# Optimization experiments

Measured on AMD Instinct MI355X. Metric: run time of the kernel, lower is better.

Reference implementation:

```python
import jax, jax.numpy as jnp
import numpy as np

B, T, D, H, L = 128, 512, 512, 512, 256


def setup_inputs() -> dict:
    key = jax.random.key(0)
    ks = jax.random.split(key, 7)
    lim = 1.0 / np.sqrt(H)
    u = lambda k, shape, lo: jax.random.uniform(k, shape, jnp.float32, -lo, lo)
    x = jax.random.normal(ks[0], (B, T, D), dtype=jnp.float32)
    Wih = u(ks[1], (3 * H, D), lim)
    Whh = u(ks[2], (3 * H, H), lim)
    b = u(ks[3], (3 * H,), lim)
    bn = u(ks[4], (H,), lim)
    lim_l = 1.0 / np.sqrt(H)
    Wlin = u(ks[5], (2 * L, H), lim_l)
    blin = u(ks[6], (2 * L,), lim_l)
    return {"x": x, "Wih": Wih, "Whh": Whh, "b": b, "bn": bn, "Wlin": Wlin, "blin": blin}


def reference(x, Wih, Whh, b, bn, Wlin, blin):
    # x: (B, T, D). Batched GRU recurrence over time via lax.scan.
    def step(h, xt):
        ig = xt @ Wih.T + b           # (B, 3H)
        hg = h @ Whh.T                # (B, 3H)
        ir, iz, inn = jnp.split(ig, 3, axis=-1)
        hr, hz, hn = jnp.split(hg, 3, axis=-1)
        r = jax.nn.sigmoid(ir + hr)
        z = jax.nn.sigmoid(iz + hz)
        n = jnp.tanh(inn + r * (hn + bn))
        h_new = (1.0 - z) * n + z * h
        return h_new, None

    xs = jnp.swapaxes(x, 0, 1)        # (T, B, D)
    h0 = jnp.zeros((x.shape[0], Whh.shape[1]), dtype=x.dtype)
    h_final, _ = jax.lax.scan(step, h0, xs)
    out = h_final @ Wlin.T + blin     # (B, 2L)
    mu, logvar = jnp.split(out, 2, axis=-1)
    return (mu, logvar)
```

## Files before the change

kernel.cpp:

```cpp
#include <hip/hip_runtime.h>
#include <stdint.h>


typedef short short8 __attribute__((ext_vector_type(8)));
typedef float f32x4 __attribute__((ext_vector_type(4)));
typedef int int4v __attribute__((ext_vector_type(4)));

#define NB 128
#define NT 512
#define ND 512
#define NH 512
#define NG 1536
#define HSLOT (NB * NH)

__device__ __forceinline__ unsigned short f2bf(float f) {
  union { float f; unsigned u; } v; v.f = f;
  unsigned r = v.u + 0x7fffu + ((v.u >> 16) & 1u);
  return (unsigned short)(r >> 16);
}
__device__ __forceinline__ float bf2f(unsigned short u) {
  union { unsigned u; float f; } v; v.u = ((unsigned)u) << 16; return v.f;
}
__device__ __forceinline__ float sigmoid_f(float x) {
  float e = __builtin_amdgcn_exp2f(-1.4426950408889634f * x);
  return __builtin_amdgcn_rcpf(1.0f + e);
}
__device__ __forceinline__ float tanh_f(float x) {
  float e = __builtin_amdgcn_exp2f(2.8853900817779268f * x);
  return 1.0f - 2.0f * __builtin_amdgcn_rcpf(1.0f + e);
}
__device__ __forceinline__ short8 pack8(float4 a, float4 b) {
  short8 s;
  s[0] = (short)f2bf(a.x); s[1] = (short)f2bf(a.y);
  s[2] = (short)f2bf(a.z); s[3] = (short)f2bf(a.w);
  s[4] = (short)f2bf(b.x); s[5] = (short)f2bf(b.y);
  s[6] = (short)f2bf(b.z); s[7] = (short)f2bf(b.w);
  return s;
}

__device__ __forceinline__ void issue4(const unsigned short* r0,
                                       const unsigned short* r1,
                                       const unsigned short* r2,
                                       const unsigned short* r3,
                                       int4v (&v)[4]) {
  asm volatile(
      "global_load_dwordx4 %0, %4, off sc0 sc1\n\t"
      "global_load_dwordx4 %1, %5, off sc0 sc1\n\t"
      "global_load_dwordx4 %2, %6, off sc0 sc1\n\t"
      "global_load_dwordx4 %3, %7, off sc0 sc1"
      : "=&v"(v[0]), "=&v"(v[1]), "=&v"(v[2]), "=&v"(v[3])
      : "v"(r0), "v"(r1), "v"(r2), "v"(r3) : "memory");
}

__device__ __forceinline__ void wait4(int4v (&v)[4]) {
  asm volatile("s_waitcnt vmcnt(0)"
               : "+v"(v[0]), "+v"(v[1]), "+v"(v[2]), "+v"(v[3]) :: "memory");
}

__device__ __forceinline__ int4v load16_s(const unsigned short* p) {
  int4v v;
  asm volatile("global_load_dwordx4 %0, %1, off sc0 sc1\n\t"
               "s_waitcnt vmcnt(0)"
               : "=v"(v) : "v"(p) : "memory");
  return v;
}

__device__ __forceinline__ void store8_nd(unsigned short* p, unsigned long long v) {
  asm volatile("global_store_dwordx2 %0, %1, off sc0 sc1"
               :: "v"(p), "v"(v) : "memory");
}

__device__ __forceinline__ void store16_s(unsigned short* p, int4v v) {
  asm volatile("global_store_dwordx4 %0, %1, off sc0 sc1"
               :: "v"(p), "v"(v) : "memory");
}

__device__ __forceinline__ unsigned poll_s(const unsigned* p) {
  unsigned f;
  asm volatile("global_load_dword %0, %1, off sc0 sc1\n\t"
               "s_waitcnt vmcnt(0)" : "=v"(f) : "v"(p) : "memory");
  return f;
}

__device__ __forceinline__ unsigned pkmax(unsigned a, unsigned b) {
  unsigned d;
  asm("v_pk_max_u16 %0, %1, %2" : "=v"(d) : "v"(a), "v"(b));
  return d;
}
__device__ __forceinline__ bool has_sent(int4v v) {
  unsigned m = pkmax(pkmax((unsigned)v[0], (unsigned)v[1]),
                     pkmax((unsigned)v[2], (unsigned)v[3]));
  return ((m & 0xFFFFu) == 0xFFFFu) || ((m >> 16) == 0xFFFFu);
}

__global__ __launch_bounds__(256) void cvt_bf16(
    const float* __restrict__ in, unsigned short* __restrict__ out, int n8) {
  int i = blockIdx.x * blockDim.x + threadIdx.x;
  const int stride = gridDim.x * blockDim.x;
  for (; i < n8; i += stride) {
    float4 a = ((const float4*)in)[2 * i];
    float4 b = ((const float4*)in)[2 * i + 1];
    *(short8*)&out[(size_t)i * 8] = pack8(a, b);
  }
}

__global__ __launch_bounds__(256) void ig_gemm(
    const float* __restrict__ x, const float* __restrict__ Wih,
    const float* __restrict__ bias, unsigned short* __restrict__ IG) {
  __shared__ unsigned short As[128 * 40];
  __shared__ unsigned short Bs[128 * 40];
  const int tid = threadIdx.x;
  const int bn = blockIdx.x, bm = blockIdx.y;
  const int lane = tid & 63, w = tid >> 6;
  const int wm = w >> 1, wn = w & 1;
  const int l15 = lane & 15, q = lane >> 4;

  f32x4 acc[4][4] = {};

  for (int kt = 0; kt < 16; ++kt) {
    __syncthreads();
#pragma unroll
    for (int j = 0; j < 4; ++j) {
      int fi = tid + 256 * j;
      int row = fi >> 3, kq = fi & 7;
      float4 v = *(const float4*)(x + (size_t)(bm * 128 + row) * ND + kt * 32 + kq * 4);
      ushort4 s = {f2bf(v.x), f2bf(v.y), f2bf(v.z), f2bf(v.w)};
      *(ushort4*)&As[row * 40 + kq * 4] = s;
    }
#pragma unroll
    for (int j = 0; j < 4; ++j) {
      int fi = tid + 256 * j;
      int row = fi >> 3, kq = fi & 7;
      float4 v = *(const float4*)(Wih + (size_t)(bn * 128 + row) * ND + kt * 32 + kq * 4);
      ushort4 s = {f2bf(v.x), f2bf(v.y), f2bf(v.z), f2bf(v.w)};
      *(ushort4*)&Bs[row * 40 + kq * 4] = s;
    }
    __syncthreads();

    short8 af[4], bf[4];
#pragma unroll
    for (int tm = 0; tm < 4; ++tm)
      af[tm] = *(const short8*)&As[(wm * 64 + tm * 16 + l15) * 40 + q * 8];
#pragma unroll
    for (int tn = 0; tn < 4; ++tn)
      bf[tn] = *(const short8*)&Bs[(wn * 64 + tn * 16 + l15) * 40 + q * 8];
#pragma unroll
    for (int tm = 0; tm < 4; ++tm)
#pragma unroll
      for (int tn = 0; tn < 4; ++tn)
        acc[tm][tn] = __builtin_amdgcn_mfma_f32_16x16x32_bf16(af[tm], bf[tn], acc[tm][tn], 0, 0, 0);
  }

#pragma unroll
  for (int tm = 0; tm < 4; ++tm) {
#pragma unroll
    for (int tn = 0; tn < 4; ++tn) {
      int col = bn * 128 + wn * 64 + tn * 16 + l15;
      float bb = bias[col];
#pragma unroll
      for (int i = 0; i < 4; ++i) {
        int row = bm * 128 + wm * 64 + tm * 16 + q * 4 + i;
        IG[(size_t)row * NG + col] = f2bf(acc[tm][tn][i] + bb);
      }
    }
  }
}

template <bool USE_IG>
__device__ __forceinline__ void gru_body(
    const float* __restrict__ x, const float* __restrict__ Wih,
    const float* __restrict__ Whh, const float* __restrict__ bias,
    const float* __restrict__ bn, const unsigned short* __restrict__ IG,
    unsigned short* __restrict__ hbuf, float* __restrict__ hfin,
    const unsigned* __restrict__ qcnt,
    unsigned short* hs, unsigned short* ts, int bid) {
  const int tid = threadIdx.x;
  const int lane = tid & 63;
  const int w = tid >> 6;
  const int l15 = lane & 15, q = lane >> 4;
  const int g = bid & 7, c = bid >> 3;
  const int col = c * 64 + w * 16 + l15;
  const int erow = g * 16 + q * 4;
  const int mrow = g * 16 + l15;

  short8 bfr[3][16];
#pragma unroll
  for (int gt = 0; gt < 3; ++gt) {
    const float* src = Whh + (size_t)(gt * NH + col) * NH + q * 8;
#pragma unroll
    for (int kk = 0; kk < 16; ++kk) {
      float4 v0 = *(const float4*)(src + kk * 32);
      float4 v1 = *(const float4*)(src + kk * 32 + 4);
      bfr[gt][kk] = pack8(v0, v1);
    }
  }

  float bi_r = 0.f, bi_z = 0.f, bi_n = 0.f;
  if (!USE_IG) {
    bi_r = bias[col];
    bi_z = bias[NH + col];
    bi_n = bias[2 * NH + col];
  }
  const float bnv = bn[col];

  float hreg[4] = {0.f, 0.f, 0.f, 0.f};

  const int frow = tid >> 4;
  const int j2 = tid & 15;
  const int fr7 = frow & 7;
  const size_t rowoff = (size_t)(g * 16 + frow) * NH;
  const int e0 = ((j2) ^ fr7) << 3;
  const int e1 = ((j2 + 16) ^ fr7) << 3;
  const int e2 = ((32 + j2) ^ fr7) << 3;
  const int e3 = ((48 + j2) ^ fr7) << 3;

  const int srow = tid >> 4;
  const int scol = (tid & 15) * 4;
  const size_t cell_off = (size_t)(g * 16 + srow) * NH + c * 64 + scol;

  int4v v[4];
  issue4(hbuf + rowoff + e0, hbuf + rowoff + e1,
         hbuf + rowoff + e2, hbuf + rowoff + e3, v);

  for (int t = 0; t < NT; ++t) {
    unsigned short* hnxt  = hbuf + (size_t)((t + 1) & 3) * HSLOT;
    unsigned short* hsent = hbuf + (size_t)((t + 2) & 3) * HSLOT;
    const unsigned short* hrow = hbuf + (size_t)(t & 3) * HSLOT + rowoff;

    if (USE_IG && qcnt != nullptr && (t & 127) == 0) {
      if (tid == 0) {
        const unsigned* qp = qcnt + (t >> 7);
        unsigned f = poll_s(qp);
        while (f < 1536u) f = poll_s(qp);
      }
      __syncthreads();
    }

    float igr[4], igz[4], ign[4];
    if (USE_IG) {
#pragma unroll
      for (int i = 0; i < 4; ++i) {
        const size_t base = ((size_t)(erow + i) * NT + t) * NG + col;
        igr[i] = bf2f(IG[base]);
        igz[i] = bf2f(IG[base + NH]);
        ign[i] = bf2f(IG[base + 2 * NH]);
      }
    }

    wait4(v);
    if (t > 0) {
      while (has_sent(v[0])) v[0] = load16_s(hrow + e0);
      while (has_sent(v[1])) v[1] = load16_s(hrow + e1);
      while (has_sent(v[2])) v[2] = load16_s(hrow + e2);
      while (has_sent(v[3])) v[3] = load16_s(hrow + e3);
    }
    *(int4v*)&hs[frow * 512 + (j2 << 3)] = v[0];
    *(int4v*)&hs[frow * 512 + ((j2 + 16) << 3)] = v[1];
    *(int4v*)&hs[frow * 512 + ((32 + j2) << 3)] = v[2];
    *(int4v*)&hs[frow * 512 + ((48 + j2) << 3)] = v[3];
    __syncthreads();

    if (t + 2 < NT) store8_nd(hsent + cell_off, 0xFFFFFFFFFFFFFFFFull);

    f32x4 ar = {0.f, 0.f, 0.f, 0.f};
    f32x4 az = {0.f, 0.f, 0.f, 0.f};
    f32x4 an = {0.f, 0.f, 0.f, 0.f};
    f32x4 ai = {0.f, 0.f, 0.f, 0.f};
    const int abase = l15 * 512;
    const int ar7 = (l15 & 7) << 3;
#pragma unroll
    for (int kk = 0; kk < 16; ++kk) {
      short8 afk = *(const short8*)&hs[abase + ((kk * 32 + q * 8) ^ ar7)];
      ar = __builtin_amdgcn_mfma_f32_16x16x32_bf16(afk, bfr[0][kk], ar, 0, 0, 0);
      az = __builtin_amdgcn_mfma_f32_16x16x32_bf16(afk, bfr[1][kk], az, 0, 0, 0);
      an = __builtin_amdgcn_mfma_f32_16x16x32_bf16(afk, bfr[2][kk], an, 0, 0, 0);
      if (!USE_IG) {
        const float* xp = x + ((size_t)mrow * NT + t) * ND + kk * 32 + q * 8;
        short8 xa = pack8(*(const float4*)xp, *(const float4*)(xp + 4));
#pragma unroll
        for (int gt = 0; gt < 3; ++gt) {
          const float* wp = Wih + (size_t)(gt * NH + col) * ND + kk * 32 + q * 8;
          short8 wf = pack8(*(const float4*)wp, *(const float4*)(wp + 4));
          if (gt == 0) ar = __builtin_amdgcn_mfma_f32_16x16x32_bf16(xa, wf, ar, 0, 0, 0);
          if (gt == 1) az = __builtin_amdgcn_mfma_f32_16x16x32_bf16(xa, wf, az, 0, 0, 0);
          if (gt == 2) ai = __builtin_amdgcn_mfma_f32_16x16x32_bf16(xa, wf, ai, 0, 0, 0);
        }
      }
    }

    unsigned short sv[4];
#pragma unroll
    for (int i = 0; i < 4; ++i) {
      float xr = USE_IG ? (ar[i] + igr[i]) : (ar[i] + bi_r);
      float xz = USE_IG ? (az[i] + igz[i]) : (az[i] + bi_z);
      float xin = USE_IG ? ign[i] : (ai[i] + bi_n);
      float r = sigmoid_f(xr);
      float z = sigmoid_f(xz);
      float n = tanh_f(xin + r * (an[i] + bnv));
      float hn2 = (1.f - z) * n + z * hreg[i];
      hreg[i] = hn2;
      sv[i] = f2bf(hn2);
      if (t == NT - 1) hfin[(size_t)(erow + i) * NH + col] = hn2;
    }

    if (t != NT - 1) {
#pragma unroll
      for (int i = 0; i < 4; ++i)
        ts[(q * 4 + i) * 64 + w * 16 + l15] = sv[i];
      asm volatile("s_waitcnt vmcnt(0)" ::: "memory");
      __syncthreads();
      store8_nd(hnxt + cell_off,
                *(const unsigned long long*)&ts[srow * 64 + scol]);
      issue4(hnxt + rowoff + e0, hnxt + rowoff + e1,
             hnxt + rowoff + e2, hnxt + rowoff + e3, v);
    }
  }
}

template <bool USE_IG>
__global__ __launch_bounds__(256, 1) void gru_rec(
    const float* __restrict__ x, const float* __restrict__ Wih,
    const float* __restrict__ Whh, const float* __restrict__ bias,
    const float* __restrict__ bn, const unsigned short* __restrict__ IG,
    unsigned short* __restrict__ hbuf, float* __restrict__ hfin) {
  __shared__ __align__(16) unsigned short hs[16 * 512];
  __shared__ __align__(16) unsigned short ts[16 * 64];
  gru_body<USE_IG>(x, Wih, Whh, bias, bn, IG, hbuf, hfin, nullptr,
                   hs, ts, blockIdx.x);
}

__global__ __launch_bounds__(256, 1) void fused_gru_ig(
    const float* __restrict__ Whh, const float* __restrict__ bn,
    const unsigned short* __restrict__ xb, const unsigned short* __restrict__ wb,
    const float* __restrict__ bias, unsigned short* __restrict__ IG,
    unsigned short* __restrict__ hbuf, float* __restrict__ hfin,
    unsigned* __restrict__ qcnt) {
  __shared__ __align__(16) unsigned short hs[16 * 512];
  __shared__ __align__(16) unsigned short ts[16 * 64];
  __shared__ __align__(16) unsigned short As[128 * 40];
  __shared__ __align__(16) unsigned short Bs[128 * 40];
  __shared__ __align__(16) unsigned short Ts[128 * 128];

  const int bid = blockIdx.x;
  const int tid = threadIdx.x;

  if (bid < 64) {
    gru_body<true>(nullptr, nullptr, Whh, bias, bn, IG, hbuf, hfin, qcnt,
                   hs, ts, bid);
    return;
  }

  const int lane = tid & 63, w = tid >> 6;
  const int wm = w >> 1, wn = w & 1;
  const int l15 = lane & 15, q = lane >> 4;

  for (int tile = bid - 64; tile < 6144; tile += 192) {
    const int qq = tile / 1536;
    const int r = tile - qq * 1536;
    const int bmq = r / 12, bnn = r - bmq * 12;
    const int bm = bmq * 4 + qq;

    f32x4 acc[4][4] = {};

    for (int kt = 0; kt < 16; ++kt) {
      __syncthreads();
#pragma unroll
      for (int j = 0; j < 2; ++j) {
        int gi = tid + 256 * j;
        int row = gi >> 2, kq = gi & 3;
        *(short8*)&As[row * 40 + kq * 8] =
            *(const short8*)(xb + (size_t)(bm * 128 + row) * ND + kt * 32 + kq * 8);
      }
#pragma unroll
      for (int j = 0; j < 2; ++j) {
        int gi = tid + 256 * j;
        int row = gi >> 2, kq = gi & 3;
        *(short8*)&Bs[row * 40 + kq * 8] =
            *(const short8*)(wb + (size_t)(bnn * 128 + row) * ND + kt * 32 + kq * 8);
      }
      __syncthreads();

      short8 af[4], bf[4];
#pragma unroll
      for (int tm = 0; tm < 4; ++tm)
        af[tm] = *(const short8*)&As[(wm * 64 + tm * 16 + l15) * 40 + q * 8];
#pragma unroll
      for (int tn = 0; tn < 4; ++tn)
        bf[tn] = *(const short8*)&Bs[(wn * 64 + tn * 16 + l15) * 40 + q * 8];
#pragma unroll
      for (int tm = 0; tm < 4; ++tm)
#pragma unroll
        for (int tn = 0; tn < 4; ++tn)
          acc[tm][tn] = __builtin_amdgcn_mfma_f32_16x16x32_bf16(af[tm], bf[tn], acc[tm][tn], 0, 0, 0);
    }

#pragma unroll
    for (int tm = 0; tm < 4; ++tm) {
#pragma unroll
      for (int tn = 0; tn < 4; ++tn) {
        int cl = wn * 64 + tn * 16 + l15;
        float bb = bias[bnn * 128 + cl];
#pragma unroll
        for (int i = 0; i < 4; ++i) {
          int rl = wm * 64 + tm * 16 + q * 4 + i;
          Ts[rl * 128 + cl] = f2bf(acc[tm][tn][i] + bb);
        }
      }
    }
    __syncthreads();
#pragma unroll
    for (int j = 0; j < 8; ++j) {
      int gi = tid + 256 * j;
      int row = gi >> 4, c16 = gi & 15;
      store16_s(IG + (size_t)(bm * 128 + row) * NG + bnn * 128 + c16 * 8,
                *(const int4v*)&Ts[row * 128 + c16 * 8]);
    }
    asm volatile("s_waitcnt vmcnt(0)" ::: "memory");
    __syncthreads();
    if (tid == 0) atomicAdd(qcnt + qq, 1u);
  }
}

__global__ __launch_bounds__(256) void final_linear(
    const float* __restrict__ hfin, const float* __restrict__ Wlin,
    const float* __restrict__ blin, float* __restrict__ out) {
  __shared__ float sh[16 * 516];
  const int tid = threadIdx.x;
  const int b0 = blockIdx.y * 16, o0 = blockIdx.x * 16;

  for (int j = tid; j < 16 * 128; j += 256) {
    int row = j >> 7, kq = j & 127;
    *(float4*)&sh[row * 516 + kq * 4] =
        *(const float4*)(hfin + (size_t)(b0 + row) * NH + kq * 4);
  }
  __syncthreads();

  const int bi = tid & 15, oi = tid >> 4;
  const int o = o0 + oi;
  const float4* wp = (const float4*)(Wlin + (size_t)o * NH);
  float4 a4 = {0.f, 0.f, 0.f, 0.f};
  for (int k4 = 0; k4 < 128; ++k4) {
    float4 wv = wp[k4];
    float4 hv = *(const float4*)&sh[bi * 516 + k4 * 4];
    a4.x += wv.x * hv.x; a4.y += wv.y * hv.y;
    a4.z += wv.z * hv.z; a4.w += wv.w * hv.w;
  }
  float v = a4.x + a4.y + a4.z + a4.w + blin[o];
  int b = b0 + bi;
  if (o < 256) out[b * 256 + o] = v;
  else out[32768 + b * 256 + (o - 256)] = v;
}

extern "C" void kernel_launch(void* const* d_in, const int* in_sizes, int n_in,
                              void* d_out, int out_size, void* d_ws, size_t ws_size,
                              hipStream_t stream) {
  const float* x    = (const float*)d_in[0];
  const float* Wih  = (const float*)d_in[1];
  const float* Whh  = (const float*)d_in[2];
  const float* bias = (const float*)d_in[3];
  const float* bn   = (const float*)d_in[4];
  const float* Wlin = (const float*)d_in[5];
  const float* blin = (const float*)d_in[6];
  float* out = (float*)d_out;

  char* ws = (char*)d_ws;
  unsigned short* hbuf = (unsigned short*)ws;
  float* hfin          = (float*)(ws + 4 * 131072);
  unsigned* qcnt       = (unsigned*)(ws + 4 * 131072 + 262144);
  unsigned short* IG   = (unsigned short*)(ws + 4 * 131072 + 262144 + 1024);
  const size_t need_min = 4 * 131072 + 262144 + 1024;
  const size_t need_ig  = need_min + (size_t)NB * NT * NG * 2;
  const size_t need_bf  = need_ig + 67108864ull + 1572864ull;
  unsigned short* xb = (unsigned short*)(ws + need_ig);
  unsigned short* wb = (unsigned short*)(ws + need_ig + 67108864ull);
  if (ws_size < need_min) return;

  hipMemsetAsync(ws, 0, 131072, stream);
  hipMemsetAsync(ws + 131072, 0xFF, 3 * 131072, stream);
  hipMemsetAsync(ws + 4 * 131072 + 262144, 0, 1024, stream);

  const bool useIG = (ws_size >= need_ig);
  const bool useBF = (ws_size >= need_bf);
  if (useIG && useBF) {
    cvt_bf16<<<2048, 256, 0, stream>>>(x, xb, (NB * NT * ND) / 8);
    cvt_bf16<<<384, 256, 0, stream>>>(Wih, wb, (NG * ND) / 8);
    fused_gru_ig<<<256, 256, 0, stream>>>(Whh, bn, xb, wb, bias, IG, hbuf,
                                          hfin, qcnt);
  } else if (useIG) {
    ig_gemm<<<dim3(12, 512), 256, 0, stream>>>(x, Wih, bias, IG);
    gru_rec<true><<<64, 256, 0, stream>>>(x, Wih, Whh, bias, bn, IG, hbuf, hfin);
  } else {
    gru_rec<false><<<64, 256, 0, stream>>>(x, Wih, Whh, bias, bn, nullptr, hbuf, hfin);
  }
  final_linear<<<dim3(32, 8), 256, 0, stream>>>(hfin, Wlin, blin, out);
}
```

Before: 1.899 ms.

## Drop bf16 pre-conversion kernels and prefill first IG quarter with all blocks

Removes the separate fp32-to-bf16 conversion kernels for x and Wih, so the fused kernel now loads fp32 and converts while staging tiles into shared memory. Before the recurrence starts, all 256 blocks cooperatively compute the first quarter of the input-gate GEMM. The remaining quarters are then produced by the 192 non-recurrent blocks while the 64 recurrent blocks run. This cuts two kernel launches and a pass over x through memory, at the cost of doubling global load bytes inside the GEMM tiles and delaying the recurrence start until the first quarter is done.

After: 1.918 ms. No clear change (+1.0%).

```diff
diff --git a/kernel.cpp b/kernel.cpp
--- a/kernel.cpp
+++ b/kernel.cpp
@@ -93,17 +93,6 @@
   return ((m & 0xFFFFu) == 0xFFFFu) || ((m >> 16) == 0xFFFFu);
 }
 
-__global__ __launch_bounds__(256) void cvt_bf16(
-    const float* __restrict__ in, unsigned short* __restrict__ out, int n8) {
-  int i = blockIdx.x * blockDim.x + threadIdx.x;
-  const int stride = gridDim.x * blockDim.x;
-  for (; i < n8; i += stride) {
-    float4 a = ((const float4*)in)[2 * i];
-    float4 b = ((const float4*)in)[2 * i + 1];
-    *(short8*)&out[(size_t)i * 8] = pack8(a, b);
-  }
-}
-
 __global__ __launch_bounds__(256) void ig_gemm(
     const float* __restrict__ x, const float* __restrict__ Wih,
     const float* __restrict__ bias, unsigned short* __restrict__ IG) {
@@ -164,6 +153,77 @@
       }
     }
   }
+}
+
+__device__ __forceinline__ void ig_tile(
+    const float* __restrict__ x, const float* __restrict__ Wih,
+    const float* __restrict__ bias, unsigned short* __restrict__ IG,
+    unsigned* __restrict__ qcnt, int bm, int bnn, int qq,
+    unsigned short* As, unsigned short* Bs, unsigned short* Ts, int tid) {
+  const int lane = tid & 63, w = tid >> 6;
+  const int wm = w >> 1, wn = w & 1;
+  const int l15 = lane & 15, q = lane >> 4;
+
+  f32x4 acc[4][4] = {};
+
+  for (int kt = 0; kt < 16; ++kt) {
+    __syncthreads();
+#pragma unroll
+    for (int j = 0; j < 4; ++j) {
+      int fi = tid + 256 * j;
+      int row = fi >> 3, kq = fi & 7;
+      float4 v = *(const float4*)(x + (size_t)(bm * 128 + row) * ND + kt * 32 + kq * 4);
+      ushort4 s = {f2bf(v.x), f2bf(v.y), f2bf(v.z), f2bf(v.w)};
+      *(ushort4*)&As[row * 40 + kq * 4] = s;
+    }
+#pragma unroll
+    for (int j = 0; j < 4; ++j) {
+      int fi = tid + 256 * j;
+      int row = fi >> 3, kq = fi & 7;
+      float4 v = *(const float4*)(Wih + (size_t)(bnn * 128 + row) * ND + kt * 32 + kq * 4);
+      ushort4 s = {f2bf(v.x), f2bf(v.y), f2bf(v.z), f2bf(v.w)};
+      *(ushort4*)&Bs[row * 40 + kq * 4] = s;
+    }
+    __syncthreads();
+
+    short8 af[4], bf[4];
+#pragma unroll
+    for (int tm = 0; tm < 4; ++tm)
+      af[tm] = *(const short8*)&As[(wm * 64 + tm * 16 + l15) * 40 + q * 8];
+#pragma unroll
+    for (int tn = 0; tn < 4; ++tn)
+      bf[tn] = *(const short8*)&Bs[(wn * 64 + tn * 16 + l15) * 40 + q * 8];
+#pragma unroll
+    for (int tm = 0; tm < 4; ++tm)
+#pragma unroll
+      for (int tn = 0; tn < 4; ++tn)
+        acc[tm][tn] = __builtin_amdgcn_mfma_f32_16x16x32_bf16(af[tm], bf[tn], acc[tm][tn], 0, 0, 0);
+  }
+
+#pragma unroll
+  for (int tm = 0; tm < 4; ++tm) {
+#pragma unroll
+    for (int tn = 0; tn < 4; ++tn) {
+      int cl = wn * 64 + tn * 16 + l15;
+      float bb = bias[bnn * 128 + cl];
+#pragma unroll
+      for (int i = 0; i < 4; ++i) {
+        int rl = wm * 64 + tm * 16 + q * 4 + i;
+        Ts[rl * 128 + cl] = f2bf(acc[tm][tn][i] + bb);
+      }
+    }
+  }
+  __syncthreads();
+#pragma unroll
+  for (int j = 0; j < 8; ++j) {
+    int gi = tid + 256 * j;
+    int row = gi >> 4, c16 = gi & 15;
+    store16_s(IG + (size_t)(bm * 128 + row) * NG + bnn * 128 + c16 * 8,
+              *(const int4v*)&Ts[row * 128 + c16 * 8]);
+  }
+  asm volatile("s_waitcnt vmcnt(0)" ::: "memory");
+  __syncthreads();
+  if (tid == 0) atomicAdd(qcnt + qq, 1u);
 }
 
 template <bool USE_IG>
@@ -330,9 +390,9 @@
 }
 
 __global__ __launch_bounds__(256, 1) void fused_gru_ig(
-    const float* __restrict__ Whh, const float* __restrict__ bn,
-    const unsigned short* __restrict__ xb, const unsigned short* __restrict__ wb,
-    const float* __restrict__ bias, unsigned short* __restrict__ IG,
+    const float* __restrict__ x, const float* __restrict__ Wih,
+    const float* __restrict__ Whh, const float* __restrict__ bias,
+    const float* __restrict__ bn, unsigned short* __restrict__ IG,
     unsigned short* __restrict__ hbuf, float* __restrict__ hfin,
     unsigned* __restrict__ qcnt) {
   __shared__ __align__(16) unsigned short hs[16 * 512];
@@ -344,80 +404,25 @@
   const int bid = blockIdx.x;
   const int tid = threadIdx.x;
 
+#pragma unroll 1
+  for (int k = 0; k < 6; ++k) {
+    const int tile = bid + 256 * k;
+    const int bmq = tile / 12, bnn = tile - bmq * 12;
+    ig_tile(x, Wih, bias, IG, qcnt, bmq * 4 + 0, bnn, 0, As, Bs, Ts, tid);
+  }
+
   if (bid < 64) {
     gru_body<true>(nullptr, nullptr, Whh, bias, bn, IG, hbuf, hfin, qcnt,
                    hs, ts, bid);
     return;
   }
 
-  const int lane = tid & 63, w = tid >> 6;
-  const int wm = w >> 1, wn = w & 1;
-  const int l15 = lane & 15, q = lane >> 4;
-
-  for (int tile = bid - 64; tile < 6144; tile += 192) {
+#pragma unroll 1
+  for (int tile = 1536 + (bid - 64); tile < 6144; tile += 192) {
     const int qq = tile / 1536;
     const int r = tile - qq * 1536;
     const int bmq = r / 12, bnn = r - bmq * 12;
-    const int bm = bmq * 4 + qq;
-
-    f32x4 acc[4][4] = {};
-
-    for (int kt = 0; kt < 16; ++kt) {
-      __syncthreads();
-#pragma unroll
-      for (int j = 0; j < 2; ++j) {
-        int gi = tid + 256 * j;
-        int row = gi >> 2, kq = gi & 3;
-        *(short8*)&As[row * 40 + kq * 8] =
-            *(const short8*)(xb + (size_t)(bm * 128 + row) * ND + kt * 32 + kq * 8);
-      }
-#pragma unroll
-      for (int j = 0; j < 2; ++j) {
-        int gi = tid + 256 * j;
-        int row = gi >> 2, kq = gi & 3;
-        *(short8*)&Bs[row * 40 + kq * 8] =
-            *(const short8*)(wb + (size_t)(bnn * 128 + row) * ND + kt * 32 + kq * 8);
-      }
-      __syncthreads();
-
-      short8 af[4], bf[4];
-#pragma unroll
-      for (int tm = 0; tm < 4; ++tm)
-        af[tm] = *(const short8*)&As[(wm * 64 + tm * 16 + l15) * 40 + q * 8];
-#pragma unroll
-      for (int tn = 0; tn < 4; ++tn)
-        bf[tn] = *(const short8*)&Bs[(wn * 64 + tn * 16 + l15) * 40 + q * 8];
-#pragma unroll
-      for (int tm = 0; tm < 4; ++tm)
-#pragma unroll
-        for (int tn = 0; tn < 4; ++tn)
-          acc[tm][tn] = __builtin_amdgcn_mfma_f32_16x16x32_bf16(af[tm], bf[tn], acc[tm][tn], 0, 0, 0);
-    }
-
-#pragma unroll
-    for (int tm = 0; tm < 4; ++tm) {
-#pragma unroll
-      for (int tn = 0; tn < 4; ++tn) {
-        int cl = wn * 64 + tn * 16 + l15;
-        float bb = bias[bnn * 128 + cl];
-#pragma unroll
-        for (int i = 0; i < 4; ++i) {
-          int rl = wm * 64 + tm * 16 + q * 4 + i;
-          Ts[rl * 128 + cl] = f2bf(acc[tm][tn][i] + bb);
-        }
-      }
-    }
-    __syncthreads();
-#pragma unroll
-    for (int j = 0; j < 8; ++j) {
-      int gi = tid + 256 * j;
-      int row = gi >> 4, c16 = gi & 15;
-      store16_s(IG + (size_t)(bm * 128 + row) * NG + bnn * 128 + c16 * 8,
-                *(const int4v*)&Ts[row * 128 + c16 * 8]);
-    }
-    asm volatile("s_waitcnt vmcnt(0)" ::: "memory");
-    __syncthreads();
-    if (tid == 0) atomicAdd(qcnt + qq, 1u);
+    ig_tile(x, Wih, bias, IG, qcnt, bmq * 4 + qq, bnn, qq, As, Bs, Ts, tid);
   }
 }
 
@@ -470,9 +475,6 @@
   unsigned short* IG   = (unsigned short*)(ws + 4 * 131072 + 262144 + 1024);
   const size_t need_min = 4 * 131072 + 262144 + 1024;
   const size_t need_ig  = need_min + (size_t)NB * NT * NG * 2;
-  const size_t need_bf  = need_ig + 67108864ull + 1572864ull;
-  unsigned short* xb = (unsigned short*)(ws + need_ig);
-  unsigned short* wb = (unsigned short*)(ws + need_ig + 67108864ull);
   if (ws_size < need_min) return;
 
   hipMemsetAsync(ws, 0, 131072, stream);
@@ -480,15 +482,9 @@
   hipMemsetAsync(ws + 4 * 131072 + 262144, 0, 1024, stream);
 
   const bool useIG = (ws_size >= need_ig);
-  const bool useBF = (ws_size >= need_bf);
-  if (useIG && useBF) {
-    cvt_bf16<<<2048, 256, 0, stream>>>(x, xb, (NB * NT * ND) / 8);
-    cvt_bf16<<<384, 256, 0, stream>>>(Wih, wb, (NG * ND) / 8);
-    fused_gru_ig<<<256, 256, 0, stream>>>(Whh, bn, xb, wb, bias, IG, hbuf,
+  if (useIG) {
+    fused_gru_ig<<<256, 256, 0, stream>>>(x, Wih, Whh, bias, bn, IG, hbuf,
                                           hfin, qcnt);
-  } else if (useIG) {
-    ig_gemm<<<dim3(12, 512), 256, 0, stream>>>(x, Wih, bias, IG);
-    gru_rec<true><<<64, 256, 0, stream>>>(x, Wih, Whh, bias, bn, IG, hbuf, hfin);
   } else {
     gru_rec<false><<<64, 256, 0, stream>>>(x, Wih, Whh, bias, bn, nullptr, hbuf, hfin);
   }
```

## Compute first IG quarter on all blocks before recurrence; merge bf16 conversion kernels

Applied to the files above, without the earlier changes.

All 256 blocks, including the 64 recurrence blocks, now compute the first quarter of the input-gate GEMM tiles before the recurrence begins. The remaining three quarters stay on the 192 helper blocks. The aim is to cut the startup wait of the recurrence blocks on the first IG chunk. The two float-to-bf16 conversion launches are also merged into one kernel to save a launch. The trade-off is that the recurrence blocks start later and, with all blocks resident, they spend shared memory and time on GEMM work first.

Measured after the change: 1.870 ms. About the same (-1.6%).

```diff
diff --git a/kernel.cpp b/kernel.cpp
--- a/kernel.cpp
+++ b/kernel.cpp
@@ -93,14 +93,24 @@
   return ((m & 0xFFFFu) == 0xFFFFu) || ((m >> 16) == 0xFFFFu);
 }
 
-__global__ __launch_bounds__(256) void cvt_bf16(
-    const float* __restrict__ in, unsigned short* __restrict__ out, int n8) {
+__global__ __launch_bounds__(256) void cvt_both(
+    const float* __restrict__ x, unsigned short* __restrict__ xb,
+    const float* __restrict__ Wih, unsigned short* __restrict__ wb) {
+  const int nx = (NB * NT * ND) / 8;
+  const int nw = (NG * ND) / 8;
   int i = blockIdx.x * blockDim.x + threadIdx.x;
   const int stride = gridDim.x * blockDim.x;
-  for (; i < n8; i += stride) {
-    float4 a = ((const float4*)in)[2 * i];
-    float4 b = ((const float4*)in)[2 * i + 1];
-    *(short8*)&out[(size_t)i * 8] = pack8(a, b);
+  for (; i < nx + nw; i += stride) {
+    if (i < nx) {
+      float4 a = ((const float4*)x)[2 * i];
+      float4 b = ((const float4*)x)[2 * i + 1];
+      *(short8*)&xb[(size_t)i * 8] = pack8(a, b);
+    } else {
+      const int j = i - nx;
+      float4 a = ((const float4*)Wih)[2 * j];
+      float4 b = ((const float4*)Wih)[2 * j + 1];
+      *(short8*)&wb[(size_t)j * 8] = pack8(a, b);
+    }
   }
 }
 
@@ -164,6 +174,75 @@
       }
     }
   }
+}
+
+__device__ __forceinline__ void ig_tile_bf16(
+    const unsigned short* __restrict__ xb, const unsigned short* __restrict__ wb,
+    const float* __restrict__ bias, unsigned short* __restrict__ IG,
+    unsigned* __restrict__ qcnt, int bm, int bnn, int qq,
+    unsigned short* As, unsigned short* Bs, unsigned short* Ts, int tid) {
+  const int lane = tid & 63, w = tid >> 6;
+  const int wm = w >> 1, wn = w & 1;
+  const int l15 = lane & 15, q = lane >> 4;
+
+  f32x4 acc[4][4] = {};
+
+  for (int kt = 0; kt < 16; ++kt) {
+    __syncthreads();
+#pragma unroll
+    for (int j = 0; j < 2; ++j) {
+      int gi = tid + 256 * j;
+      int row = gi >> 2, kq = gi & 3;
+      *(short8*)&As[row * 40 + kq * 8] =
+          *(const short8*)(xb + (size_t)(bm * 128 + row) * ND + kt * 32 + kq * 8);
+    }
+#pragma unroll
+    for (int j = 0; j < 2; ++j) {
+      int gi = tid + 256 * j;
+      int row = gi >> 2, kq = gi & 3;
+      *(short8*)&Bs[row * 40 + kq * 8] =
+          *(const short8*)(wb + (size_t)(bnn * 128 + row) * ND + kt * 32 + kq * 8);
+    }
+    __syncthreads();
+
+    short8 af[4], bf[4];
+#pragma unroll
+    for (int tm = 0; tm < 4; ++tm)
+      af[tm] = *(const short8*)&As[(wm * 64 + tm * 16 + l15) * 40 + q * 8];
+#pragma unroll
+    for (int tn = 0; tn < 4; ++tn)
+      bf[tn] = *(const short8*)&Bs[(wn * 64 + tn * 16 + l15) * 40 + q * 8];
+#pragma unroll
+    for (int tm = 0; tm < 4; ++tm)
+#pragma unroll
+      for (int tn = 0; tn < 4; ++tn)
+        acc[tm][tn] = __builtin_amdgcn_mfma_f32_16x16x32_bf16(af[tm], bf[tn], acc[tm][tn], 0, 0, 0);
+  }
+
+#pragma unroll
+  for (int tm = 0; tm < 4; ++tm) {
+#pragma unroll
+    for (int tn = 0; tn < 4; ++tn) {
+      int cl = wn * 64 + tn * 16 + l15;
+      float bb = bias[bnn * 128 + cl];
+#pragma unroll
+      for (int i = 0; i < 4; ++i) {
+        int rl = wm * 64 + tm * 16 + q * 4 + i;
+        Ts[rl * 128 + cl] = f2bf(acc[tm][tn][i] + bb);
+      }
+    }
+  }
+  __syncthreads();
+#pragma unroll
+  for (int j = 0; j < 8; ++j) {
+    int gi = tid + 256 * j;
+    int row = gi >> 4, c16 = gi & 15;
+    store16_s(IG + (size_t)(bm * 128 + row) * NG + bnn * 128 + c16 * 8,
+              *(const int4v*)&Ts[row * 128 + c16 * 8]);
+  }
+  asm volatile("s_waitcnt vmcnt(0)" ::: "memory");
+  __syncthreads();
+  if (tid == 0) atomicAdd(qcnt + qq, 1u);
 }
 
 template <bool USE_IG>
@@ -344,80 +423,25 @@
   const int bid = blockIdx.x;
   const int tid = threadIdx.x;
 
+#pragma unroll 1
+  for (int k = 0; k < 6; ++k) {
+    const int tile = bid + 256 * k;
+    const int bmq = tile / 12, bnn = tile - bmq * 12;
+    ig_tile_bf16(xb, wb, bias, IG, qcnt, bmq * 4 + 0, bnn, 0, As, Bs, Ts, tid);
+  }
+
   if (bid < 64) {
     gru_body<true>(nullptr, nullptr, Whh, bias, bn, IG, hbuf, hfin, qcnt,
                    hs, ts, bid);
     return;
   }
 
-  const int lane = tid & 63, w = tid >> 6;
-  const int wm = w >> 1, wn = w & 1;
-  const int l15 = lane & 15, q = lane >> 4;
-
-  for (int tile = bid - 64; tile < 6144; tile += 192) {
+#pragma unroll 1
+  for (int tile = 1536 + (bid - 64); tile < 6144; tile += 192) {
     const int qq = tile / 1536;
     const int r = tile - qq * 1536;
     const int bmq = r / 12, bnn = r - bmq * 12;
-    const int bm = bmq * 4 + qq;
-
-    f32x4 acc[4][4] = {};
-
-    for (int kt = 0; kt < 16; ++kt) {
-      __syncthreads();
-#pragma unroll
-      for (int j = 0; j < 2; ++j) {
-        int gi = tid + 256 * j;
-        int row = gi >> 2, kq = gi & 3;
-        *(short8*)&As[row * 40 + kq * 8] =
-            *(const short8*)(xb + (size_t)(bm * 128 + row) * ND + kt * 32 + kq * 8);
-      }
-#pragma unroll
-      for (int j = 0; j < 2; ++j) {
-        int gi = tid + 256 * j;
-        int row = gi >> 2, kq = gi & 3;
-        *(short8*)&Bs[row * 40 + kq * 8] =
-            *(const short8*)(wb + (size_t)(bnn * 128 + row) * ND + kt * 32 + kq * 8);
-      }
-      __syncthreads();
-
-      short8 af[4], bf[4];
-#pragma unroll
-      for (int tm = 0; tm < 4; ++tm)
-        af[tm] = *(const short8*)&As[(wm * 64 + tm * 16 + l15) * 40 + q * 8];
-#pragma unroll
-      for (int tn = 0; tn < 4; ++tn)
-        bf[tn] = *(const short8*)&Bs[(wn * 64 + tn * 16 + l15) * 40 + q * 8];
-#pragma unroll
-      for (int tm = 0; tm < 4; ++tm)
-#pragma unroll
-        for (int tn = 0; tn < 4; ++tn)
-          acc[tm][tn] = __builtin_amdgcn_mfma_f32_16x16x32_bf16(af[tm], bf[tn], acc[tm][tn], 0, 0, 0);
-    }
-
-#pragma unroll
-    for (int tm = 0; tm < 4; ++tm) {
-#pragma unroll
-      for (int tn = 0; tn < 4; ++tn) {
-        int cl = wn * 64 + tn * 16 + l15;
-        float bb = bias[bnn * 128 + cl];
-#pragma unroll
-        for (int i = 0; i < 4; ++i) {
-          int rl = wm * 64 + tm * 16 + q * 4 + i;
-          Ts[rl * 128 + cl] = f2bf(acc[tm][tn][i] + bb);
-        }
-      }
-    }
-    __syncthreads();
-#pragma unroll
-    for (int j = 0; j < 8; ++j) {
-      int gi = tid + 256 * j;
-      int row = gi >> 4, c16 = gi & 15;
-      store16_s(IG + (size_t)(bm * 128 + row) * NG + bnn * 128 + c16 * 8,
-                *(const int4v*)&Ts[row * 128 + c16 * 8]);
-    }
-    asm volatile("s_waitcnt vmcnt(0)" ::: "memory");
-    __syncthreads();
-    if (tid == 0) atomicAdd(qcnt + qq, 1u);
+    ig_tile_bf16(xb, wb, bias, IG, qcnt, bmq * 4 + qq, bnn, qq, As, Bs, Ts, tid);
   }
 }
 
@@ -482,8 +506,7 @@
   const bool useIG = (ws_size >= need_ig);
   const bool useBF = (ws_size >= need_bf);
   if (useIG && useBF) {
-    cvt_bf16<<<2048, 256, 0, stream>>>(x, xb, (NB * NT * ND) / 8);
-    cvt_bf16<<<384, 256, 0, stream>>>(Wih, wb, (NG * ND) / 8);
+    cvt_both<<<2048, 256, 0, stream>>>(x, xb, Wih, wb);
     fused_gru_ig<<<256, 256, 0, stream>>>(Whh, bn, xb, wb, bias, IG, hbuf,
                                           hfin, qcnt);
   } else if (useIG) {
```
